# Performance work log

Hardware: AMD Instinct MI355X
Metric: run time of the kernel (lower is better)

The kernel has to match this reference:

```python
import jax, jax.numpy as jnp
import numpy as np

E = 1024  # embed_dim
H = 16    # num_heads
D = E // H  # head_dim


def setup_inputs() -> dict:
    key = jax.random.key(0)
    ks = jax.random.split(key, 9)
    s = 0.02
    return {
        "hidden_state": jax.random.normal(ks[0], (4, 1024, E), jnp.float32),
        "Wq": jax.random.normal(ks[1], (H, D, E), jnp.float32) * s,
        "bq": jax.random.normal(ks[2], (H, D), jnp.float32) * s,
        "Wk": jax.random.normal(ks[3], (H, D, E), jnp.float32) * s,
        "bk": jax.random.normal(ks[4], (H, D), jnp.float32) * s,
        "Wv": jax.random.normal(ks[5], (H, D, E), jnp.float32) * s,
        "bv": jax.random.normal(ks[6], (H, D), jnp.float32) * s,
        "Wo": jax.random.normal(ks[7], (E, E), jnp.float32) * s,
        "bo": jax.random.normal(ks[8], (E,), jnp.float32) * s,
    }


def _mha(x, Wq, bq, Wk, bk, Wv, bv, Wo, bo):
    # Per-head linear projections (torch Linear: y = x W^T + b), batched over heads.
    q = jnp.einsum("bse,hde->bhsd", x, Wq) + bq[None, :, None, :]
    k = jnp.einsum("bse,hde->bhsd", x, Wk) + bk[None, :, None, :]
    v = jnp.einsum("bse,hde->bhsd", x, Wv) + bv[None, :, None, :]
    scores = jnp.einsum("bhsd,bhtd->bhst", q, k) / jnp.sqrt(jnp.asarray(D, x.dtype))
    w = jax.nn.softmax(scores, axis=-1)  # F.softmax default -> last dim
    o = jnp.einsum("bhst,bhtd->bhsd", w, v)
    # concat heads along last dim: [B,S,H*D] in head order (matches torch.cat)
    B, _, S, _ = o.shape
    o = jnp.transpose(o, (0, 2, 1, 3)).reshape(B, S, H * D)
    return o @ Wo.T + bo


def reference(hidden_state, Wq, bq, Wk, bk, Wv, bv, Wo, bo):
    return _mha(hidden_state, Wq, bq, Wk, bk, Wv, bv, Wo, bo)
```

## Files before the change

### kernel.cpp

```cpp
#include <hip/hip_runtime.h>
#include <hip/hip_bf16.h>
#include <stdint.h>

#define E_DIM 1024
#define H_NUM 16
#define D_DIM 64
#define B_NUM 4
#define S_LEN 1024

typedef __attribute__((ext_vector_type(8))) short bf16x8;
typedef __attribute__((ext_vector_type(4))) short bf16x4;
typedef __attribute__((ext_vector_type(4))) float f32x4;

#define SOFTMAX_C2 0.18033688011112042f

__device__ inline ushort f2b(float x) {
    __hip_bfloat16 h = __float2bfloat16(x);
    return *(ushort*)&h;
}
__device__ inline float b2f(ushort u) {
    __hip_bfloat16 h = *(__hip_bfloat16*)&u;
    return __bfloat162float(h);
}
__device__ inline uint pk2(float a, float b) {
    __hip_bfloat162 h = __float22bfloat162_rn(make_float2(a, b));
    return *(uint*)&h;
}

__device__ inline void gld16(const ushort* g, ushort* l) {
    __builtin_amdgcn_global_load_lds((const __attribute__((address_space(1))) void*)g,
                                     (__attribute__((address_space(3))) void*)l, 16, 0, 0);
}

__global__ __launch_bounds__(256)
void convert_all(const float* __restrict__ X,  const float* __restrict__ Wq,
                 const float* __restrict__ Wk, const float* __restrict__ Wv,
                 const float* __restrict__ Wo,
                 ushort* __restrict__ Xb, ushort* __restrict__ Wcat,
                 ushort* __restrict__ Wob)
{
    const int bid = blockIdx.x;
    const float* src; ushort* dst; size_t off;
    if (bid < 4096)      { src = X;  dst = Xb;   off = (size_t)bid * 1024; }
    else if (bid < 5120) { src = Wq; dst = Wcat;              off = (size_t)(bid - 4096) * 1024; }
    else if (bid < 6144) { src = Wk; dst = Wcat + (1u << 20); off = (size_t)(bid - 5120) * 1024; }
    else if (bid < 7168) { src = Wv; dst = Wcat + (2u << 20); off = (size_t)(bid - 6144) * 1024; }
    else                 { src = Wo; dst = Wob;               off = (size_t)(bid - 7168) * 1024; }
    const size_t i = off + (size_t)threadIdx.x * 4;
    float4 v = *(const float4*)&src[i];
    ushort4 o;
    o.x = f2b(v.x); o.y = f2b(v.y); o.z = f2b(v.z); o.w = f2b(v.w);
    *(ushort4*)&dst[i] = o;
}

__global__ __launch_bounds__(256)
void gemm_qkv(const ushort* __restrict__ A, const ushort* __restrict__ Bw,
              const float* __restrict__ b0, const float* __restrict__ b1,
              const float* __restrict__ b2,
              ushort* __restrict__ Qb, ushort* __restrict__ Kb,
              ushort* __restrict__ Vt_g, int K)
{
    __shared__ __align__(16) ushort SM[12288];
    ushort* As = SM;
    ushort* Bs = SM + 8192;

    const int tid  = threadIdx.x;
    const int wave = tid >> 6;
    const int lane = tid & 63;
    const int quad = lane >> 4;
    const int l16  = lane & 15;
    const int wm   = wave & 1;
    const int wn   = wave >> 1;
    const int m0   = blockIdx.x * 128;
    const int n0   = blockIdx.y * 64;

    f32x4 acc[4][2] = {};

#pragma unroll
    for (int i = 0; i < 2; ++i) {
        const int e = i * 256 + tid;
        gld16(&A[(size_t)(m0 + (e >> 2)) * K + (e & 3) * 8], &As[e * 8]);
    }
    gld16(&Bw[(size_t)(n0 + (tid >> 2)) * K + (tid & 3) * 8], &Bs[tid * 8]);
    __syncthreads();

    const int nk = K >> 5;
    for (int ki = 0; ki < nk; ++ki) {
        const int cur = ki & 1;
        if (ki + 1 < nk) {
            const int k0 = (ki + 1) << 5;
#pragma unroll
            for (int i = 0; i < 2; ++i) {
                const int e = i * 256 + tid;
                gld16(&A[(size_t)(m0 + (e >> 2)) * K + k0 + (e & 3) * 8],
                      &As[(cur ^ 1) * 4096 + e * 8]);
            }
            gld16(&Bw[(size_t)(n0 + (tid >> 2)) * K + k0 + (tid & 3) * 8],
                  &Bs[(cur ^ 1) * 2048 + tid * 8]);
        }

        bf16x8 af[4], bf[2];
#pragma unroll
        for (int mi = 0; mi < 4; ++mi)
            af[mi] = *(const bf16x8*)&As[cur * 4096 + (wm * 64 + mi * 16 + l16) * 32 + quad * 8];
#pragma unroll
        for (int ni = 0; ni < 2; ++ni)
            bf[ni] = *(const bf16x8*)&Bs[cur * 2048 + (wn * 32 + ni * 16 + l16) * 32 + quad * 8];
#pragma unroll
        for (int mi = 0; mi < 4; ++mi)
#pragma unroll
            for (int ni = 0; ni < 2; ++ni)
                acc[mi][ni] = __builtin_amdgcn_mfma_f32_16x16x32_bf16(af[mi], bf[ni], acc[mi][ni], 0, 0, 0);
        __syncthreads();
    }

    const int seg   = n0 >> 10;
    const int cbase = n0 & 1023;
    const float* bp = (seg == 0) ? b0 : (seg == 1) ? b1 : b2;
    const float scl = (seg == 0) ? SOFTMAX_C2 : 1.0f;

    if (seg < 2) {
        ushort* T = SM;
#pragma unroll
        for (int ni = 0; ni < 2; ++ni) {
            const int nloc = wn * 32 + ni * 16 + l16;
            const float bv = bp[cbase + nloc];
#pragma unroll
            for (int mi = 0; mi < 4; ++mi)
#pragma unroll
                for (int r = 0; r < 4; ++r)
                    T[(wm * 64 + mi * 16 + quad * 4 + r) * 72 + nloc] =
                        f2b((acc[mi][ni][r] + bv) * scl);
        }
        __syncthreads();
        ushort* dst = (seg == 0) ? Qb : Kb;
        const int row = tid >> 1, half = tid & 1;
        const ushort* s = &T[row * 72 + half * 32];
        ushort* d = &dst[(size_t)(m0 + row) * 1024 + cbase + half * 32];
#pragma unroll
        for (int j = 0; j < 4; ++j)
            *(uint4*)(d + j * 8) = *(const uint4*)(s + j * 8);
    } else {
        ushort* Tt = SM;
        const int hh = cbase >> 6;
        const int b  = m0 >> 10, sbase = m0 & 1023;
#pragma unroll
        for (int ni = 0; ni < 2; ++ni) {
            const int nloc = wn * 32 + ni * 16 + l16;
            const float bv = bp[cbase + nloc];
#pragma unroll
            for (int mi = 0; mi < 4; ++mi) {
                const int mloc = wm * 64 + mi * 16 + quad * 4;
                ushort4 pk;
                pk.x = f2b(acc[mi][ni][0] + bv);
                pk.y = f2b(acc[mi][ni][1] + bv);
                pk.z = f2b(acc[mi][ni][2] + bv);
                pk.w = f2b(acc[mi][ni][3] + bv);
                *(ushort4*)&Tt[nloc * 136 + mloc] = pk;
            }
        }
        __syncthreads();
        const int nrow = tid >> 2, qtr = tid & 3;
        const ushort* s = &Tt[nrow * 136 + qtr * 32];
        ushort* d = &Vt_g[(((size_t)(b * 16 + hh)) * 64 + nrow) * 1024 + sbase + qtr * 32];
#pragma unroll
        for (int j = 0; j < 4; ++j)
            *(uint4*)(d + j * 8) = *(const uint4*)(s + j * 8);
    }
}

__global__ __launch_bounds__(256)
void attention6(const ushort* __restrict__ Qg, const ushort* __restrict__ Kg,
                const ushort* __restrict__ Vg,
                ushort* __restrict__ Opart, float* __restrict__ Lpart)
{
    __shared__ ushort Kb[2][32][72];
    __shared__ ushort Vb[2][64][40];

    const int tid  = threadIdx.x;
    const int w    = tid >> 6;
    const int lane = tid & 63;
    const int quad = lane >> 4;
    const int l16  = lane & 15;

    const int qt = blockIdx.x;
    const int bh = blockIdx.y;
    const int th = blockIdx.z;
    const int b  = bh >> 4;
    const int h  = bh & 15;
    const size_t tbase = ((size_t)b * S_LEN) * E_DIM + (size_t)h * D_DIM;
    const size_t vbase = (size_t)bh * D_DIM * S_LEN;
    const int t0 = th * 512;

    const ushort* qrow = Qg + tbase + (size_t)(qt * 64 + w * 16 + l16) * E_DIM + quad * 8;
    bf16x8 qf[2];
    qf[0] = *(const bf16x8*)qrow;
    qf[1] = *(const bf16x8*)(qrow + 32);

    {
        const int kr = tid >> 3, kc = (tid & 7) * 8;
        *(uint4*)&Kb[0][kr][kc] = *(const uint4*)&Kg[tbase + (size_t)(t0 + kr) * E_DIM + kc];
        const int vr = tid >> 2, vc = (tid & 3) * 8;
        *(uint4*)&Vb[0][vr][vc] = *(const uint4*)&Vg[vbase + (size_t)vr * S_LEN + t0 + vc];
    }
    __syncthreads();

    float lq = 0.0f;
    f32x4 oacc[4] = {};

    for (int kt = 0; kt < 16; ++kt) {
        const int cur = kt & 1;

        uint4 kpre, vpre;
        const int kr = tid >> 3, kc = (tid & 7) * 8;
        const int vr = tid >> 2, vc = (tid & 3) * 8;
        if (kt < 15) {
            const int tg = t0 + (kt + 1) * 32;
            kpre = *(const uint4*)&Kg[tbase + (size_t)(tg + kr) * E_DIM + kc];
            vpre = *(const uint4*)&Vg[vbase + (size_t)vr * S_LEN + tg + vc];
        }

        f32x4 sacc[2] = {};
#pragma unroll
        for (int mt = 0; mt < 2; ++mt)
#pragma unroll
            for (int ks = 0; ks < 2; ++ks) {
                bf16x8 kf = *(const bf16x8*)&Kb[cur][mt * 16 + l16][ks * 32 + quad * 8];
                sacc[mt] = __builtin_amdgcn_mfma_f32_16x16x32_bf16(kf, qf[ks], sacc[mt], 0, 0, 0);
            }

        bf16x4 pf[2];
        float rs = 0.0f;
#pragma unroll
        for (int mt = 0; mt < 2; ++mt) {
            float p0 = exp2f(sacc[mt][0]);
            float p1 = exp2f(sacc[mt][1]);
            float p2 = exp2f(sacc[mt][2]);
            float p3 = exp2f(sacc[mt][3]);
            rs += (p0 + p1) + (p2 + p3);
            union { uint uu[2]; bf16x4 v; } pk;
            pk.uu[0] = pk2(p0, p1);
            pk.uu[1] = pk2(p2, p3);
            pf[mt] = pk.v;
        }
        lq += rs;

#pragma unroll
        for (int nb = 0; nb < 4; ++nb)
#pragma unroll
            for (int kb = 0; kb < 2; ++kb) {
                bf16x4 vf = *(const bf16x4*)&Vb[cur][nb * 16 + l16][kb * 16 + quad * 4];
                oacc[nb] = __builtin_amdgcn_mfma_f32_16x16x16bf16_1k(pf[kb], vf, oacc[nb], 0, 0, 0);
            }

        if (kt < 15) {
            const int nxt = cur ^ 1;
            *(uint4*)&Kb[nxt][kr][kc] = kpre;
            *(uint4*)&Vb[nxt][vr][vc] = vpre;
        }
        __syncthreads();
    }

    lq += __shfl_xor(lq, 16);
    lq += __shfl_xor(lq, 32);
    const size_t obase = ((size_t)(th * 64 + bh)) * S_LEN;
    if (lane < 16)
        Lpart[obase + qt * 64 + w * 16 + l16] = lq;

    ushort* T = &Kb[0][0][0];
#pragma unroll
    for (int nb = 0; nb < 4; ++nb)
#pragma unroll
        for (int r = 0; r < 4; ++r)
            T[(w * 16 + quad * 4 + r) * 72 + nb * 16 + l16] = f2b(oacc[nb][r]);
    __syncthreads();
    {
        const int row = tid >> 2, c16 = (tid & 3) * 16;
        const ushort* s = &T[row * 72 + c16];
        ushort* d = &Opart[(obase + qt * 64 + row) * 64 + c16];
        *(uint4*)(d)     = *(const uint4*)(s);
        *(uint4*)(d + 8) = *(const uint4*)(s + 8);
    }
}

__global__ __launch_bounds__(256)
void combine(const ushort* __restrict__ Opart, const float* __restrict__ Lpart,
             ushort* __restrict__ AO)
{
    const int bh = blockIdx.x >> 6;
    const int qc = blockIdx.x & 63;
    const int b  = bh >> 4;
    const int h  = bh & 15;
    const int q  = qc * 16 + (threadIdx.x >> 4);
    const int d4 = (threadIdx.x & 15) * 4;

    const size_t i0 = (((size_t)bh) * S_LEN + q) * 64 + d4;
    const size_t i1 = (((size_t)(64 + bh)) * S_LEN + q) * 64 + d4;
    ushort4 o0 = *(const ushort4*)&Opart[i0];
    ushort4 o1 = *(const ushort4*)&Opart[i1];
    const float l0 = Lpart[(size_t)bh * S_LEN + q];
    const float l1 = Lpart[(size_t)(64 + bh) * S_LEN + q];
    const float li = 1.0f / (l0 + l1);

    union { uint uu[2]; ushort4 v; } r;
    r.uu[0] = pk2((b2f(o0.x) + b2f(o1.x)) * li, (b2f(o0.y) + b2f(o1.y)) * li);
    r.uu[1] = pk2((b2f(o0.z) + b2f(o1.z)) * li, (b2f(o0.w) + b2f(o1.w)) * li);
    AO[((size_t)(b * S_LEN + q)) * E_DIM + h * 64 + d4] = r.v.x;
    *(ushort4*)&AO[((size_t)(b * S_LEN + q)) * E_DIM + h * 64 + d4] = r.v;
}

__global__ __launch_bounds__(256)
void gemm_out(const ushort* __restrict__ A, const ushort* __restrict__ Bw,
              const float* __restrict__ bias, float* __restrict__ Cout, int K)
{
    __shared__ __align__(16) ushort SM[8704];
    ushort* As = SM;
    ushort* Bs = SM + 4096;

    const int tid  = threadIdx.x;
    const int w    = tid >> 6;
    const int lane = tid & 63;
    const int quad = lane >> 4;
    const int l16  = lane & 15;
    const int m0   = blockIdx.x * 64;
    const int n0   = blockIdx.y * 64;

    f32x4 acc[4] = {};

    gld16(&A[(size_t)(m0 + (tid >> 2)) * K + (tid & 3) * 8], &As[tid * 8]);
    gld16(&Bw[(size_t)(n0 + (tid >> 2)) * K + (tid & 3) * 8], &Bs[tid * 8]);
    __syncthreads();

    const int nk = K >> 5;
    for (int ki = 0; ki < nk; ++ki) {
        const int cur = ki & 1;
        if (ki + 1 < nk) {
            const int k0 = (ki + 1) << 5;
            gld16(&A[(size_t)(m0 + (tid >> 2)) * K + k0 + (tid & 3) * 8],
                  &As[(cur ^ 1) * 2048 + tid * 8]);
            gld16(&Bw[(size_t)(n0 + (tid >> 2)) * K + k0 + (tid & 3) * 8],
                  &Bs[(cur ^ 1) * 2048 + tid * 8]);
        }
        bf16x8 af = *(const bf16x8*)&As[cur * 2048 + (w * 16 + l16) * 32 + quad * 8];
#pragma unroll
        for (int nb = 0; nb < 4; ++nb) {
            bf16x8 bf = *(const bf16x8*)&Bs[cur * 2048 + (nb * 16 + l16) * 32 + quad * 8];
            acc[nb] = __builtin_amdgcn_mfma_f32_16x16x32_bf16(af, bf, acc[nb], 0, 0, 0);
        }
        __syncthreads();
    }

    float* Tf = (float*)SM;
#pragma unroll
    for (int nb = 0; nb < 4; ++nb) {
        const float bv = bias[n0 + nb * 16 + l16];
#pragma unroll
        for (int r = 0; r < 4; ++r)
            Tf[(w * 16 + quad * 4 + r) * 68 + nb * 16 + l16] = acc[nb][r] + bv;
    }
    __syncthreads();
    {
        const int row = tid >> 2, c16 = (tid & 3) * 16;
        const float* s = &Tf[row * 68 + c16];
        float* d = &Cout[(size_t)(m0 + row) * 1024 + n0 + c16];
#pragma unroll
        for (int j = 0; j < 4; ++j)
            *(float4*)(d + j * 4) = *(const float4*)(s + j * 4);
    }
}

extern "C" void kernel_launch(void* const* d_in, const int* in_sizes, int n_in,
                              void* d_out, int out_size, void* d_ws, size_t ws_size,
                              hipStream_t stream)
{
    (void)in_sizes; (void)n_in; (void)out_size; (void)ws_size;

    const float* X  = (const float*)d_in[0];
    const float* Wq = (const float*)d_in[1];
    const float* bq = (const float*)d_in[2];
    const float* Wk = (const float*)d_in[3];
    const float* bk = (const float*)d_in[4];
    const float* Wv = (const float*)d_in[5];
    const float* bv = (const float*)d_in[6];
    const float* Wo = (const float*)d_in[7];
    const float* bo = (const float*)d_in[8];

    const size_t MEG = 1u << 20;
    ushort* ws    = (ushort*)d_ws;
    ushort* Xb    = ws;
    ushort* Wcat  = ws + 4 * MEG;
    ushort* Wob   = ws + 7 * MEG;
    ushort* Qb    = ws + 8 * MEG;
    ushort* Kb    = ws + 12 * MEG;
    ushort* Vtg   = ws + 16 * MEG;
    ushort* Opart = ws + 20 * MEG;
    float*  Lpart = (float*)(ws + 28 * MEG);
    ushort* AO    = Xb;

    dim3 blk(256);

    convert_all<<<8192, blk, 0, stream>>>(X, Wq, Wk, Wv, Wo, Xb, Wcat, Wob);

    gemm_qkv<<<dim3(32, 48), blk, 0, stream>>>(Xb, Wcat, bq, bk, bv,
                                               Qb, Kb, Vtg, E_DIM);

    attention6<<<dim3(16, 64, 2), blk, 0, stream>>>(Qb, Kb, Vtg, Opart, Lpart);

    combine<<<4096, blk, 0, stream>>>(Opart, Lpart, AO);

    gemm_out<<<dim3(64, 16), blk, 0, stream>>>(AO, Wob, bo, (float*)d_out, E_DIM);
}
```

Baseline: 203.3 us.

## Fuse split-K attention combine into output GEMM and widen GEMM K-tiles

The separate combine kernel is removed: the output projection GEMM now reads the two partial attention outputs and their softmax denominators directly, merges and normalizes them in registers, and writes the bf16 A-tile to shared memory while the current tile computes. The QKV GEMM and output GEMM move to a 64-wide K step with XOR-swizzled shared memory to cut bank conflicts and halve barrier count, and the output GEMM uses 128x64 tiles. Launch-bounds occupancy hints are added. This saves one launch and the intermediate AO round-trip, at the cost of extra register pressure and larger shared memory per block.

```diff
diff --git a/kernel.cpp b/kernel.cpp
--- a/kernel.cpp
+++ b/kernel.cpp
@@ -53,16 +53,16 @@
     *(ushort4*)&dst[i] = o;
 }
 
-__global__ __launch_bounds__(256)
+__global__ __launch_bounds__(256, 3)
 void gemm_qkv(const ushort* __restrict__ A, const ushort* __restrict__ Bw,
               const float* __restrict__ b0, const float* __restrict__ b1,
               const float* __restrict__ b2,
               ushort* __restrict__ Qb, ushort* __restrict__ Kb,
               ushort* __restrict__ Vt_g, int K)
 {
-    __shared__ __align__(16) ushort SM[12288];
+    __shared__ __align__(16) ushort SM[24576];
     ushort* As = SM;
-    ushort* Bs = SM + 8192;
+    ushort* Bs = SM + 16384;
 
     const int tid  = threadIdx.x;
     const int wave = tid >> 6;
@@ -76,41 +76,50 @@
 
     f32x4 acc[4][2] = {};
 
-#pragma unroll
-    for (int i = 0; i < 2; ++i) {
-        const int e = i * 256 + tid;
-        gld16(&A[(size_t)(m0 + (e >> 2)) * K + (e & 3) * 8], &As[e * 8]);
-    }
-    gld16(&Bw[(size_t)(n0 + (tid >> 2)) * K + (tid & 3) * 8], &Bs[tid * 8]);
+    auto stageA = [&](int buf, int k0) {
+#pragma unroll
+        for (int i = 0; i < 4; ++i) {
+            const int e   = i * 256 + tid;
+            const int row = e >> 3;
+            const int gc8 = ((e & 7) ^ (row & 7)) * 8;
+            gld16(&A[(size_t)(m0 + row) * K + k0 + gc8], &As[buf * 8192 + e * 8]);
+        }
+    };
+    auto stageB = [&](int buf, int k0) {
+#pragma unroll
+        for (int i = 0; i < 2; ++i) {
+            const int e   = i * 256 + tid;
+            const int row = e >> 3;
+            const int gc8 = ((e & 7) ^ (row & 7)) * 8;
+            gld16(&Bw[(size_t)(n0 + row) * K + k0 + gc8], &Bs[buf * 4096 + e * 8]);
+        }
+    };
+
+    stageA(0, 0); stageB(0, 0);
     __syncthreads();
 
-    const int nk = K >> 5;
+    const int nk = K >> 6;
+    const int xa = (l16 & 7) * 8;
     for (int ki = 0; ki < nk; ++ki) {
         const int cur = ki & 1;
-        if (ki + 1 < nk) {
-            const int k0 = (ki + 1) << 5;
-#pragma unroll
-            for (int i = 0; i < 2; ++i) {
-                const int e = i * 256 + tid;
-                gld16(&A[(size_t)(m0 + (e >> 2)) * K + k0 + (e & 3) * 8],
-                      &As[(cur ^ 1) * 4096 + e * 8]);
-            }
-            gld16(&Bw[(size_t)(n0 + (tid >> 2)) * K + k0 + (tid & 3) * 8],
-                  &Bs[(cur ^ 1) * 2048 + tid * 8]);
-        }
-
-        bf16x8 af[4], bf[2];
-#pragma unroll
-        for (int mi = 0; mi < 4; ++mi)
-            af[mi] = *(const bf16x8*)&As[cur * 4096 + (wm * 64 + mi * 16 + l16) * 32 + quad * 8];
-#pragma unroll
-        for (int ni = 0; ni < 2; ++ni)
-            bf[ni] = *(const bf16x8*)&Bs[cur * 2048 + (wn * 32 + ni * 16 + l16) * 32 + quad * 8];
-#pragma unroll
-        for (int mi = 0; mi < 4; ++mi)
+        if (ki + 1 < nk) { stageA(cur ^ 1, (ki + 1) << 6); stageB(cur ^ 1, (ki + 1) << 6); }
+
+#pragma unroll
+        for (int ks = 0; ks < 2; ++ks) {
+            const int lc = (ks * 32 + quad * 8) ^ xa;
+            bf16x8 af[4], bf[2];
+#pragma unroll
+            for (int mi = 0; mi < 4; ++mi)
+                af[mi] = *(const bf16x8*)&As[cur * 8192 + (wm * 64 + mi * 16 + l16) * 64 + lc];
 #pragma unroll
             for (int ni = 0; ni < 2; ++ni)
-                acc[mi][ni] = __builtin_amdgcn_mfma_f32_16x16x32_bf16(af[mi], bf[ni], acc[mi][ni], 0, 0, 0);
+                bf[ni] = *(const bf16x8*)&Bs[cur * 4096 + (wn * 32 + ni * 16 + l16) * 64 + lc];
+#pragma unroll
+            for (int mi = 0; mi < 4; ++mi)
+#pragma unroll
+                for (int ni = 0; ni < 2; ++ni)
+                    acc[mi][ni] = __builtin_amdgcn_mfma_f32_16x16x32_bf16(af[mi], bf[ni], acc[mi][ni], 0, 0, 0);
+        }
         __syncthreads();
     }
 
@@ -169,7 +178,7 @@
     }
 }
 
-__global__ __launch_bounds__(256)
+__global__ __launch_bounds__(256, 8)
 void attention6(const ushort* __restrict__ Qg, const ushort* __restrict__ Kg,
                 const ushort* __restrict__ Vg,
                 ushort* __restrict__ Opart, float* __restrict__ Lpart)
@@ -283,89 +292,135 @@
     }
 }
 
-__global__ __launch_bounds__(256)
-void combine(const ushort* __restrict__ Opart, const float* __restrict__ Lpart,
-             ushort* __restrict__ AO)
+__global__ __launch_bounds__(256, 3)
+void gemm_out(const ushort* __restrict__ Opart, const float* __restrict__ Lpart,
+              const ushort* __restrict__ Bw, const float* __restrict__ bias,
+              float* __restrict__ Cout)
 {
-    const int bh = blockIdx.x >> 6;
-    const int qc = blockIdx.x & 63;
-    const int b  = bh >> 4;
-    const int h  = bh & 15;
-    const int q  = qc * 16 + (threadIdx.x >> 4);
-    const int d4 = (threadIdx.x & 15) * 4;
-
-    const size_t i0 = (((size_t)bh) * S_LEN + q) * 64 + d4;
-    const size_t i1 = (((size_t)(64 + bh)) * S_LEN + q) * 64 + d4;
-    ushort4 o0 = *(const ushort4*)&Opart[i0];
-    ushort4 o1 = *(const ushort4*)&Opart[i1];
-    const float l0 = Lpart[(size_t)bh * S_LEN + q];
-    const float l1 = Lpart[(size_t)(64 + bh) * S_LEN + q];
-    const float li = 1.0f / (l0 + l1);
-
-    union { uint uu[2]; ushort4 v; } r;
-    r.uu[0] = pk2((b2f(o0.x) + b2f(o1.x)) * li, (b2f(o0.y) + b2f(o1.y)) * li);
-    r.uu[1] = pk2((b2f(o0.z) + b2f(o1.z)) * li, (b2f(o0.w) + b2f(o1.w)) * li);
-    AO[((size_t)(b * S_LEN + q)) * E_DIM + h * 64 + d4] = r.v.x;
-    *(ushort4*)&AO[((size_t)(b * S_LEN + q)) * E_DIM + h * 64 + d4] = r.v;
-}
-
-__global__ __launch_bounds__(256)
-void gemm_out(const ushort* __restrict__ A, const ushort* __restrict__ Bw,
-              const float* __restrict__ bias, float* __restrict__ Cout, int K)
-{
-    __shared__ __align__(16) ushort SM[8704];
+    __shared__ __align__(16) ushort SM[26624];
     ushort* As = SM;
-    ushort* Bs = SM + 4096;
+    ushort* Bs = SM + 18432;
 
     const int tid  = threadIdx.x;
-    const int w    = tid >> 6;
+    const int wave = tid >> 6;
     const int lane = tid & 63;
     const int quad = lane >> 4;
     const int l16  = lane & 15;
-    const int m0   = blockIdx.x * 64;
+    const int wm   = wave & 1;
+    const int wn   = wave >> 1;
+    const int m0   = blockIdx.x * 128;
     const int n0   = blockIdx.y * 64;
 
-    f32x4 acc[4] = {};
-
-    gld16(&A[(size_t)(m0 + (tid >> 2)) * K + (tid & 3) * 8], &As[tid * 8]);
-    gld16(&Bw[(size_t)(n0 + (tid >> 2)) * K + (tid & 3) * 8], &Bs[tid * 8]);
+    const int arow = tid >> 1;
+    const int ah   = (tid & 1) * 32;
+    const int m    = m0 + arow;
+    const int ab   = m >> 10;
+    const int as   = m & 1023;
+
+    f32x4 acc[4][2] = {};
+
+    auto loadA = [&](int ki, uint4* o0, uint4* o1, float* linv) {
+        const int bh = ab * 16 + ki;
+        const size_t p0 = ((size_t)bh * 1024 + as) * 64 + ah;
+        const size_t p1 = ((size_t)(64 + bh) * 1024 + as) * 64 + ah;
+#pragma unroll
+        for (int j = 0; j < 4; ++j) {
+            o0[j] = *(const uint4*)&Opart[p0 + j * 8];
+            o1[j] = *(const uint4*)&Opart[p1 + j * 8];
+        }
+        const float l0 = Lpart[(size_t)bh * 1024 + as];
+        const float l1 = Lpart[(size_t)(64 + bh) * 1024 + as];
+        *linv = 1.0f / (l0 + l1);
+    };
+    auto writeA = [&](int buf, const uint4* o0, const uint4* o1, float linv) {
+        ushort* dst = &As[buf * 9216 + arow * 72 + ah];
+#pragma unroll
+        for (int j = 0; j < 4; ++j) {
+            const ushort* a = (const ushort*)&o0[j];
+            const ushort* c = (const ushort*)&o1[j];
+            union { uint uu[4]; uint4 v; } pk;
+            pk.uu[0] = pk2((b2f(a[0]) + b2f(c[0])) * linv, (b2f(a[1]) + b2f(c[1])) * linv);
+            pk.uu[1] = pk2((b2f(a[2]) + b2f(c[2])) * linv, (b2f(a[3]) + b2f(c[3])) * linv);
+            pk.uu[2] = pk2((b2f(a[4]) + b2f(c[4])) * linv, (b2f(a[5]) + b2f(c[5])) * linv);
+            pk.uu[3] = pk2((b2f(a[6]) + b2f(c[6])) * linv, (b2f(a[7]) + b2f(c[7])) * linv);
+            *(uint4*)(dst + j * 8) = pk.v;
+        }
+    };
+    auto stageB = [&](int buf, int k0) {
+#pragma unroll
+        for (int i = 0; i < 2; ++i) {
+            const int e   = i * 256 + tid;
+            const int row = e >> 3;
+            const int gc8 = ((e & 7) ^ (row & 7)) * 8;
+            gld16(&Bw[(size_t)(n0 + row) * 1024 + k0 + gc8], &Bs[buf * 4096 + e * 8]);
+        }
+    };
+
+    {
+        uint4 o0[4], o1[4]; float linv;
+        loadA(0, o0, o1, &linv);
+        writeA(0, o0, o1, linv);
+        stageB(0, 0);
+    }
     __syncthreads();
 
-    const int nk = K >> 5;
-    for (int ki = 0; ki < nk; ++ki) {
+    const int xa = (l16 & 7) * 8;
+    for (int ki = 0; ki < 16; ++ki) {
         const int cur = ki & 1;
-        if (ki + 1 < nk) {
-            const int k0 = (ki + 1) << 5;
-            gld16(&A[(size_t)(m0 + (tid >> 2)) * K + k0 + (tid & 3) * 8],
-                  &As[(cur ^ 1) * 2048 + tid * 8]);
-            gld16(&Bw[(size_t)(n0 + (tid >> 2)) * K + k0 + (tid & 3) * 8],
-                  &Bs[(cur ^ 1) * 2048 + tid * 8]);
-        }
-        bf16x8 af = *(const bf16x8*)&As[cur * 2048 + (w * 16 + l16) * 32 + quad * 8];
-#pragma unroll
-        for (int nb = 0; nb < 4; ++nb) {
-            bf16x8 bf = *(const bf16x8*)&Bs[cur * 2048 + (nb * 16 + l16) * 32 + quad * 8];
-            acc[nb] = __builtin_amdgcn_mfma_f32_16x16x32_bf16(af, bf, acc[nb], 0, 0, 0);
-        }
+
+        uint4 o0[4], o1[4]; float linv;
+        if (ki + 1 < 16) {
+            loadA(ki + 1, o0, o1, &linv);
+            stageB(cur ^ 1, (ki + 1) << 6);
+        }
+
+#pragma unroll
+        for (int ks = 0; ks < 2; ++ks) {
+            const int lcB = (ks * 32 + quad * 8) ^ xa;
+            bf16x8 af[4], bf[2];
+#pragma unroll
+            for (int mi = 0; mi < 4; ++mi)
+                af[mi] = *(const bf16x8*)&As[cur * 9216 + (wm * 64 + mi * 16 + l16) * 72 + ks * 32 + quad * 8];
+#pragma unroll
+            for (int ni = 0; ni < 2; ++ni)
+                bf[ni] = *(const bf16x8*)&Bs[cur * 4096 + (wn * 32 + ni * 16 + l16) * 64 + lcB];
+#pragma unroll
+            for (int mi = 0; mi < 4; ++mi)
+#pragma unroll
+                for (int ni = 0; ni < 2; ++ni)
+                    acc[mi][ni] = __builtin_amdgcn_mfma_f32_16x16x32_bf16(af[mi], bf[ni], acc[mi][ni], 0, 0, 0);
+        }
+
+        if (ki + 1 < 16) writeA(cur ^ 1, o0, o1, linv);
         __syncthreads();
     }
 
     float* Tf = (float*)SM;
-#pragma unroll
-    for (int nb = 0; nb < 4; ++nb) {
-        const float bv = bias[n0 + nb * 16 + l16];
-#pragma unroll
-        for (int r = 0; r < 4; ++r)
-            Tf[(w * 16 + quad * 4 + r) * 68 + nb * 16 + l16] = acc[nb][r] + bv;
-    }
-    __syncthreads();
-    {
+    float bv[2];
+#pragma unroll
+    for (int ni = 0; ni < 2; ++ni)
+        bv[ni] = bias[n0 + wn * 32 + ni * 16 + l16];
+#pragma unroll
+    for (int p = 0; p < 2; ++p) {
+        if (wm == p) {
+#pragma unroll
+            for (int ni = 0; ni < 2; ++ni) {
+                const int nloc = wn * 32 + ni * 16 + l16;
+#pragma unroll
+                for (int mi = 0; mi < 4; ++mi)
+#pragma unroll
+                    for (int r = 0; r < 4; ++r)
+                        Tf[(mi * 16 + quad * 4 + r) * 68 + nloc] = acc[mi][ni][r] + bv[ni];
+            }
+        }
+        __syncthreads();
         const int row = tid >> 2, c16 = (tid & 3) * 16;
         const float* s = &Tf[row * 68 + c16];
-        float* d = &Cout[(size_t)(m0 + row) * 1024 + n0 + c16];
+        float* d = &Cout[(size_t)(m0 + p * 64 + row) * 1024 + n0 + c16];
 #pragma unroll
         for (int j = 0; j < 4; ++j)
             *(float4*)(d + j * 4) = *(const float4*)(s + j * 4);
+        __syncthreads();
     }
 }
 
@@ -395,7 +450,6 @@
     ushort* Vtg   = ws + 16 * MEG;
     ushort* Opart = ws + 20 * MEG;
     float*  Lpart = (float*)(ws + 28 * MEG);
-    ushort* AO    = Xb;
 
     dim3 blk(256);
 
@@ -406,7 +460,6 @@
 
     attention6<<<dim3(16, 64, 2), blk, 0, stream>>>(Qb, Kb, Vtg, Opart, Lpart);
 
-    combine<<<4096, blk, 0, stream>>>(Opart, Lpart, AO);
-
-    gemm_out<<<dim3(64, 16), blk, 0, stream>>>(AO, Wob, bo, (float*)d_out, E_DIM);
-}
+    gemm_out<<<dim3(32, 16), blk, 0, stream>>>(Opart, Lpart, Wob, bo,
+                                               (float*)d_out);
+}
```

Result: no change. 201.5 us (-0.9%).
